# Kernel tuning notes

Hardware: AMD Instinct MI355X
Metric: run time of the kernel (lower is better)

The kernel has to match this reference:

```python
import jax, jax.numpy as jnp
import numpy as np

ALPHA = 0.2
NEG = -9e15


def _gru(x, Wih, Whh, bih, bhh):
    # x: [B, T, F]; PyTorch nn.GRU cell equations, scan over time.
    H = Whh.shape[1]
    xg = jnp.einsum('btf,gf->btg', x, Wih) + bih  # [B,T,3H]

    def step(h, gi):
        gh = h @ Whh.T + bhh
        ir, iz, inn = jnp.split(gi, 3, axis=-1)
        hr, hz, hn = jnp.split(gh, 3, axis=-1)
        r = jax.nn.sigmoid(ir + hr)
        z = jax.nn.sigmoid(iz + hz)
        n = jnp.tanh(inn + r * hn)
        h = (1.0 - z) * n + z * h
        return h, h

    h0 = jnp.zeros((x.shape[0], H), x.dtype)
    _, ys = jax.lax.scan(step, h0, jnp.swapaxes(xg, 0, 1))
    return jnp.swapaxes(ys, 0, 1)  # [B,T,H]


def _gru_attn(x, Wih, Whh, bih, bhh, aw, ab):
    out = _gru(x, Wih, Whh, bih, bhh)              # [B,T,H]
    w = jax.nn.softmax(out @ aw + ab, axis=1)       # [B,T,1]
    return jnp.sum(out * w, axis=1)                 # [B,H]


def _gat(h, mask, W, a):
    # GraphAttentionLayer with concat=True: elu(softmax(mask(leakyrelu(Wh1+Wh2^T))) @ Wh)
    Wh = h @ W                                      # [N,O]
    O = W.shape[1]
    e = jax.nn.leaky_relu((Wh @ a[:O]) + (Wh @ a[O:]).T, ALPHA)  # [N,N]
    att = jax.nn.softmax(jnp.where(mask, e, NEG), axis=1)
    return jax.nn.elu(att @ Wh)


def setup_inputs() -> dict:
    key = jax.random.key(0)
    ks = iter(jax.random.split(key, 40))
    B, S, Wk, D, F = 1, 2048, 32, 5, 16
    H, E, NS = 128, 128, 16

    def rn(shape, scale=0.1):
        return jax.random.normal(next(ks), shape, jnp.float32) * scale

    inp = {
        'stock_features': jax.random.normal(next(ks), (B, S, Wk, D, F), jnp.float32),
        'stock_to_sector': jax.random.randint(next(ks), (S,), 0, NS, jnp.int32),
        'inter_adj': jax.random.randint(next(ks), (NS, NS), 0, 2, jnp.int32),
        'gru1_Wih': rn((3 * H, F)), 'gru1_Whh': rn((3 * H, H)),
        'gru1_bih': rn((3 * H,)), 'gru1_bhh': rn((3 * H,)),
        'attn1_w': rn((H, 1)), 'attn1_b': rn((1,)),
        'gat_intra_W': rn((H, E)), 'gat_intra_a': rn((2 * E, 1)),
        'grug_Wih': rn((3 * E, E)), 'grug_Whh': rn((3 * E, E)),
        'grug_bih': rn((3 * E,)), 'grug_bhh': rn((3 * E,)),
        'attng_w': rn((E, 1)), 'attng_b': rn((1,)),
        'grua_Wih': rn((3 * E, H)), 'grua_Whh': rn((3 * E, E)),
        'grua_bih': rn((3 * E,)), 'grua_bhh': rn((3 * E,)),
        'attna_w': rn((E, 1)), 'attna_b': rn((1,)),
        'gat_inter_W': rn((E, E)), 'gat_inter_a': rn((2 * E, 1)),
        'fusion_w': rn((3 * E, E)), 'fusion_b': rn((E,)),
        'ret_w': rn((E, 1)), 'ret_b': rn((1,)),
        'mov_w': rn((E, 1)), 'mov_b': rn((1,)),
    }
    return inp


def reference(stock_features, stock_to_sector, inter_adj,
              gru1_Wih, gru1_Whh, gru1_bih, gru1_bhh, attn1_w, attn1_b,
              gat_intra_W, gat_intra_a,
              grug_Wih, grug_Whh, grug_bih, grug_bhh, attng_w, attng_b,
              grua_Wih, grua_Whh, grua_bih, grua_bhh, attna_w, attna_b,
              gat_inter_W, gat_inter_a,
              fusion_w, fusion_b, ret_w, ret_b, mov_w, mov_b):
    B, S, Wk, D, F = stock_features.shape
    H = gru1_Whh.shape[1]
    E = gat_intra_W.shape[1]
    NS = inter_adj.shape[0]

    # Short-term: GRU-attention over days, vectorized over (batch, stock, week).
    x = stock_features.reshape(B * S * Wk, D, F)
    short = _gru_attn(x, gru1_Wih, gru1_Whh, gru1_bih, gru1_bhh, attn1_w, attn1_b)
    short = short.reshape(B, S, Wk, H)

    # Intra-sector GAT on last-week embeddings; per-sector softmax == block mask.
    same_sector = stock_to_sector[:, None] == stock_to_sector[None, :]  # [S,S]
    last = short[:, :, -1, :]                                            # [B,S,H]
    intra = jax.vmap(lambda h: _gat(h, same_sector, gat_intra_W, gat_intra_a))(last)  # [B,S,E]

    # Long-term GRU-attentions.
    lg = _gru_attn(intra.reshape(B * S, 1, E), grug_Wih, grug_Whh, grug_bih, grug_bhh,
                   attng_w, attng_b).reshape(B, S, E)
    la = _gru_attn(short.reshape(B * S, Wk, H), grua_Wih, grua_Whh, grua_bih, grua_bhh,
                   attna_w, attna_b).reshape(B, S, E)

    # Sector embeddings = mean of stock long-term embeddings per sector.
    def sector_mean(g):
        sums = jax.ops.segment_sum(g, stock_to_sector, num_segments=NS)
        cnt = jax.ops.segment_sum(jnp.ones((g.shape[0], 1), g.dtype),
                                  stock_to_sector, num_segments=NS)
        return sums / jnp.maximum(cnt, 1.0)

    sec = jax.vmap(sector_mean)(lg)                                      # [B,NS,E]
    imask = inter_adj > 0
    sec_out = jax.vmap(lambda h: _gat(h, imask, gat_inter_W, gat_inter_a))(sec)
    sec_ps = sec_out[:, stock_to_sector, :]                               # [B,S,E]

    fused = jnp.concatenate([lg, la, sec_ps], axis=-1) @ fusion_w + fusion_b
    returns = (fused @ ret_w + ret_b)[..., 0]
    moves = jax.nn.sigmoid(fused @ mov_w + mov_b)[..., 0]
    return jnp.stack([returns, moves])  # [2,B,S]
```

## Files before the change

kernel.cpp:

```cpp
#include <hip/hip_runtime.h>
#include <math.h>

#define LRELU_A 0.2f
#define NEGBIG (-9.0e15f)

typedef _Float16 f16;
typedef _Float16 f16x8 __attribute__((ext_vector_type(8)));
typedef _Float16 f16x4 __attribute__((ext_vector_type(4)));
typedef float floatx4 __attribute__((ext_vector_type(4)));

__device__ __forceinline__ float rcpf(float x){ return __builtin_amdgcn_rcpf(x); }
__device__ __forceinline__ float sigm(float x){ return rcpf(1.0f+__expf(-x)); }
__device__ __forceinline__ float gru_fuse(float xr, float xz, float xn_pre, float ghn, float h){
    float Er = __expf(-xr);
    float r  = rcpf(1.0f + Er);
    float En = __expf(2.0f*(xn_pre + r*ghn));
    float Ez = __expf(-xz);
    float Dn = En + 1.0f;
    float num = fmaf(h, Dn, (En - 1.0f)*Ez);
    float den = Dn * (1.0f + Ez);
    return num * rcpf(den);
}
__device__ __forceinline__ f16x8 load_cvt8(const float* __restrict__ p){
    float4 a = *(const float4*)p; float4 b = *(const float4*)(p+4);
    f16x8 r; r[0]=(f16)a.x; r[1]=(f16)a.y; r[2]=(f16)a.z; r[3]=(f16)a.w;
    r[4]=(f16)b.x; r[5]=(f16)b.y; r[6]=(f16)b.z; r[7]=(f16)b.w;
    return r;
}
#define MFMA16(A,B,C) __builtin_amdgcn_mfma_f32_16x16x32_f16((A),(B),(C),0,0,0)

__global__ __launch_bounds__(256) void prep_kernel(
    const float* __restrict__ g1Wih, const float* __restrict__ g1Whh,
    const float* __restrict__ gaWih, const float* __restrict__ gaWhh,
    const float* __restrict__ giW,   const float* __restrict__ fw,
    const int* __restrict__ sec,
    f16* __restrict__ Wcat1, f16* __restrict__ WcatA,
    f16* __restrict__ WT, f16* __restrict__ fwT,
    int* __restrict__ memflat, int* __restrict__ pos,
    int* __restrict__ cnt, int* __restrict__ base)
{
    __shared__ int cs[16], wsc[16];
    const int b = blockIdx.x, tid = threadIdx.x;
    if (b < 160){
        for (int idx = b*256+tid; idx < 512*160; idx += 160*256){
            int r = idx/160, k = idx - r*160;
            float v = 0.0f;
            if (r < 256){ if (k < 32){ if (k < 16) v = g1Wih[r*16+k]; } else v = g1Whh[r*128 + (k-32)]; }
            else if (r < 384){ if (k < 16) v = g1Wih[r*16+k]; }
            else { if (k >= 32) v = g1Whh[(r-128)*128 + (k-32)]; }
            Wcat1[idx] = (f16)v;
        }
    } else if (b < 416){
        for (int idx = (b-160)*256+tid; idx < 512*256; idx += 256*256){
            int r = idx >> 8, k = idx & 255;
            float v = 0.0f;
            if (r < 256){ v = (k < 128) ? gaWih[r*128+k] : gaWhh[r*128 + (k-128)]; }
            else if (r < 384){ if (k < 128) v = gaWih[r*128+k]; }
            else { if (k >= 128) v = gaWhh[(r-128)*128 + (k-128)]; }
            WcatA[idx] = (f16)v;
        }
    } else if (b < 480){
        int idx = (b-416)*256+tid;
        int r = idx >> 7, c = idx & 127;
        WT[c*128 + r] = (f16)giW[idx];
    } else if (b < 672){
        int idx = (b-480)*256+tid;
        int r = idx >> 7, c = idx & 127;
        fwT[c*384 + r] = (f16)fw[idx];
    } else {
        if (tid < 16) cs[tid] = 0;
        __syncthreads();
        for (int s = tid; s < 2048; s += 256) atomicAdd(&cs[sec[s]], 1);
        __syncthreads();
        if (tid == 0){
            int acc = 0;
            for (int g=0; g<16; g++){ cnt[g]=cs[g]; base[g]=acc; wsc[g]=acc; acc+=cs[g]; }
        }
        __syncthreads();
        for (int s = tid; s < 2048; s += 256){
            int g = sec[s];
            int p = atomicAdd(&wsc[g], 1);
            memflat[p] = s;
            pos[s] = p;
        }
    }
}

__global__ __launch_bounds__(512,2) void gru_short(
    const float* __restrict__ x, const f16* __restrict__ Wcat,
    const float* __restrict__ bih, const float* __restrict__ bhh,
    const float* __restrict__ aw, const float* __restrict__ ab,
    f16* __restrict__ out)
{
    __shared__ __align__(16) f16 xs[5][32][40];
    __shared__ __align__(16) f16 hs[2][32][136];
    __shared__ float scpart[2][8][32];
    const int tid = threadIdx.x, w = tid>>6, lane = tid&63;
    const int c = lane&15, quad = lane>>4;
    const int s0 = blockIdx.x*32;

    { f16x4 z4 = {0,0,0,0};
      f16x4* zx = (f16x4*)&xs[0][0][0];
      for (int i=tid; i<1600; i+=512) zx[i] = z4;
      f16x4* zh = (f16x4*)&hs[1][0][0];
      for (int i=tid; i<1088; i+=512) zh[i] = z4; }
    for (int i=tid; i<640; i+=512){
        int s = i/20, q = i - 20*s;
        float4 v = *(const float4*)&x[(size_t)(s0+s)*80 + q*4];
        int t = (q*4)>>4, f = (q*4)&15;
        f16x4 h4; h4[0]=(f16)v.x; h4[1]=(f16)v.y; h4[2]=(f16)v.z; h4[3]=(f16)v.w;
        *(f16x4*)&xs[t][s][f] = h4;
    }
    const int jrow = w*16 + c;
    f16x8 Ar[5], Az[5], Agi, Agh[4];
#pragma unroll
    for (int kb=0;kb<5;kb++){
        Ar[kb] = *(const f16x8*)&Wcat[(size_t)(jrow)*160 + kb*32 + quad*8];
        Az[kb] = *(const f16x8*)&Wcat[(size_t)(128+jrow)*160 + kb*32 + quad*8];
    }
    Agi = *(const f16x8*)&Wcat[(size_t)(256+jrow)*160 + quad*8];
#pragma unroll
    for (int i=0;i<4;i++)
        Agh[i] = *(const f16x8*)&Wcat[(size_t)(384+jrow)*160 + 32 + i*32 + quad*8];

    float brz_r[4], brz_z[4], b_in[4], b_hn[4], awr[4];
#pragma unroll
    for (int r=0;r<4;r++){
        int j = w*16 + quad*4 + r;
        brz_r[r] = bih[j] + bhh[j];
        brz_z[r] = bih[128+j] + bhh[128+j];
        b_in[r] = bih[256+j]; b_hn[r] = bhh[256+j];
        awr[r] = aw[j];
    }
    const float abv = ab[0];
    float hreg[2][4], aacc[2][4], l_[2] = {0.0f, 0.0f};
#pragma unroll
    for (int st=0; st<2; st++)
#pragma unroll
        for (int r=0;r<4;r++){ hreg[st][r]=0.0f; aacc[st][r]=0.0f; }
    __syncthreads();

#pragma unroll 1
    for (int t=0; t<5; ++t){
        const int rp = (t&1)^1, wp = t&1;
        f16x8 Bx[2], Bh[2][4];
#pragma unroll
        for (int st=0; st<2; st++){
            Bx[st] = *(const f16x8*)&xs[t][st*16+c][quad*8];
#pragma unroll
            for (int i=0;i<4;i++)
                Bh[st][i] = *(const f16x8*)&hs[rp][st*16+c][i*32+quad*8];
        }
        if (t > 0){
#pragma unroll
            for (int st=0; st<2; st++){
                float sc = abv;
#pragma unroll
                for (int ww=0; ww<8; ww++) sc += scpart[rp][ww][st*16+c];
                float e = __expf(sc);
                l_[st] += e;
#pragma unroll
                for (int r=0;r<4;r++) aacc[st][r] += e*hreg[st][r];
            }
        }
        float sp[2];
#pragma unroll
        for (int st=0; st<2; st++){
            floatx4 ar = {0,0,0,0}, az = {0,0,0,0}, agi = {0,0,0,0}, agh = {0,0,0,0};
            ar = MFMA16(Ar[0], Bx[st], ar);
            az = MFMA16(Az[0], Bx[st], az);
            agi = MFMA16(Agi, Bx[st], agi);
#pragma unroll
            for (int i=0;i<4;i++){
                ar = MFMA16(Ar[1+i], Bh[st][i], ar);
                az = MFMA16(Az[1+i], Bh[st][i], az);
                agh = MFMA16(Agh[i], Bh[st][i], agh);
            }
            f16x4 h4;
            sp[st] = 0.0f;
#pragma unroll
            for (int r=0;r<4;r++){
                float hn = gru_fuse(ar[r] + brz_r[r], az[r] + brz_z[r],
                                    agi[r] + b_in[r], agh[r] + b_hn[r], hreg[st][r]);
                hreg[st][r] = hn; h4[r] = (f16)hn;
                sp[st] += hn * awr[r];
            }
            *(f16x4*)&hs[wp][st*16 + c][w*16 + quad*4] = h4;
        }
#pragma unroll
        for (int st=0; st<2; st++){
            sp[st] += __shfl_xor(sp[st], 16);
            sp[st] += __shfl_xor(sp[st], 32);
        }
        if (lane < 16){ scpart[wp][w][lane] = sp[0]; scpart[wp][w][16+lane] = sp[1]; }
        __syncthreads();
    }
#pragma unroll
    for (int st=0; st<2; st++){
        float sc = abv;
#pragma unroll
        for (int ww=0; ww<8; ww++) sc += scpart[0][ww][st*16+c];
        float e = __expf(sc);
        l_[st] += e;
        float inv = rcpf(l_[st]);
        f16x4 h4;
#pragma unroll
        for (int r=0;r<4;r++) h4[r] = (f16)((aacc[st][r] + e*hreg[st][r])*inv);
        *(f16x4*)&hs[0][st*16 + c][w*16 + quad*4] = h4;
    }
    __syncthreads();
    { int s = tid>>4, p = tid&15;
      *(f16x8*)&out[(size_t)(s0+s)*128 + p*8] = *(const f16x8*)&hs[0][s][p*8]; }
}

__global__ __launch_bounds__(512,2) void gru_la(
    const f16* __restrict__ xseq, const f16* __restrict__ Wcat,
    const float* __restrict__ bih, const float* __restrict__ bhh,
    const float* __restrict__ aw, const float* __restrict__ ab,
    f16* __restrict__ out)
{
    __shared__ __align__(16) f16 xs[2][16][136];
    __shared__ __align__(16) f16 hs[2][16][136];
    __shared__ float scpart[2][8][16];
    const int tid = threadIdx.x, w = tid>>6, lane = tid&63;
    const int c = lane&15, quad = lane>>4;
    const int s0 = blockIdx.x*8;

    { f16x4 z4 = {0,0,0,0};
      f16x4* za = (f16x4*)&xs[0][0][0];
      for (int i=tid; i<1088; i+=512) za[i] = z4;
      f16x4* zh = (f16x4*)&hs[0][0][0];
      for (int i=tid; i<1088; i+=512) zh[i] = z4; }
    __syncthreads();
    if (tid < 128){
        int s = tid>>4, p = tid&15;
        *(f16x8*)&xs[0][s][p*8] = *(const f16x8*)&xseq[((size_t)(s0+s)*32 + 0)*128 + p*8];
    }
    const int jrow = w*16 + c;
    f16x8 Ar[8], Az[8], Agi[4], Agh[4];
#pragma unroll
    for (int kb=0;kb<8;kb++){
        Ar[kb] = *(const f16x8*)&Wcat[(size_t)(jrow)*256 + kb*32 + quad*8];
        Az[kb] = *(const f16x8*)&Wcat[(size_t)(128+jrow)*256 + kb*32 + quad*8];
    }
#pragma unroll
    for (int i=0;i<4;i++){
        Agi[i] = *(const f16x8*)&Wcat[(size_t)(256+jrow)*256 + i*32 + quad*8];
        Agh[i] = *(const f16x8*)&Wcat[(size_t)(384+jrow)*256 + 128 + i*32 + quad*8];
    }
    float brz_r[4], brz_z[4], b_in[4], b_hn[4], awr[4];
#pragma unroll
    for (int r=0;r<4;r++){
        int j = w*16 + quad*4 + r;
        brz_r[r] = bih[j] + bhh[j];
        brz_z[r] = bih[128+j] + bhh[128+j];
        b_in[r] = bih[256+j]; b_hn[r] = bhh[256+j];
        awr[r] = aw[j];
    }
    const float abv = ab[0];
    float hreg[4] = {0,0,0,0}, aacc[4] = {0,0,0,0}, l_ = 0.0f;
    __syncthreads();

#pragma unroll 1
    for (int t=0; t<32; ++t){
        const int rp = (t&1)^1, wp = t&1, xp = t&1;
        f16x8 Bx[4], Bh[4];
#pragma unroll
        for (int i=0;i<4;i++){
            Bx[i] = *(const f16x8*)&xs[xp][c][i*32+quad*8];
            Bh[i] = *(const f16x8*)&hs[rp][c][i*32+quad*8];
        }
        f16x8 xstage;
        const bool do_stage = (t < 31) && (tid < 128);
        if (do_stage){
            int s = tid>>4, p = tid&15;
            xstage = *(const f16x8*)&xseq[((size_t)(s0+s)*32 + t+1)*128 + p*8];
        }
        if (t > 0){
            float sc = abv;
#pragma unroll
            for (int ww=0; ww<8; ww++) sc += scpart[rp][ww][c];
            float e = __expf(sc);
            l_ += e;
#pragma unroll
            for (int r=0;r<4;r++) aacc[r] += e*hreg[r];
        }
        floatx4 ar = {0,0,0,0}, az = {0,0,0,0}, agi = {0,0,0,0}, agh = {0,0,0,0};
#pragma unroll
        for (int i=0;i<4;i++){
            ar = MFMA16(Ar[i], Bx[i], ar);
            az = MFMA16(Az[i], Bx[i], az);
            agi = MFMA16(Agi[i], Bx[i], agi);
        }
#pragma unroll
        for (int i=0;i<4;i++){
            ar = MFMA16(Ar[4+i], Bh[i], ar);
            az = MFMA16(Az[4+i], Bh[i], az);
            agh = MFMA16(Agh[i], Bh[i], agh);
        }
        f16x4 h4;
        float sp = 0.0f;
#pragma unroll
        for (int r=0;r<4;r++){
            float hn = gru_fuse(ar[r] + brz_r[r], az[r] + brz_z[r],
                                agi[r] + b_in[r], agh[r] + b_hn[r], hreg[r]);
            hreg[r] = hn; h4[r] = (f16)hn;
            sp += hn * awr[r];
        }
        *(f16x4*)&hs[wp][c][w*16 + quad*4] = h4;
        if (do_stage){
            int s = tid>>4, p = tid&15;
            *(f16x8*)&xs[xp^1][s][p*8] = xstage;
        }
        sp += __shfl_xor(sp, 16);
        sp += __shfl_xor(sp, 32);
        if (lane < 16) scpart[wp][w][lane] = sp;
        __syncthreads();
    }
    {
        float sc = abv;
#pragma unroll
        for (int ww=0; ww<8; ww++) sc += scpart[1][ww][c];
        float e = __expf(sc);
        l_ += e;
        float inv = rcpf(l_);
        f16x4 h4;
#pragma unroll
        for (int r=0;r<4;r++) h4[r] = (f16)((aacc[r] + e*hreg[r])*inv);
        *(f16x4*)&hs[1][c][w*16 + quad*4] = h4;
    }
    __syncthreads();
    if (tid < 128){
        int s = tid>>4, p = tid&15;
        *(f16x8*)&out[(size_t)(s0+s)*128 + p*8] = *(const f16x8*)&hs[1][s][p*8];
    }
}

__global__ __launch_bounds__(256) void gat_prep(
    const f16* __restrict__ shrt16, const f16* __restrict__ WT,
    const float* __restrict__ gia, const int* __restrict__ memflat,
    f16* __restrict__ Whs, float* __restrict__ ers, float* __restrict__ el)
{
    __shared__ __align__(16) float tbuf[32][132];
    __shared__ int rows[32];
    const int tid = threadIdx.x, w = tid>>6, lane = tid&63;
    const int c = lane&15, quad = lane>>4;
    const int p0 = blockIdx.x*32;
    if (tid < 32) rows[tid] = memflat[p0 + tid];
    __syncthreads();
    f16x8 A[2][4];
#pragma unroll
    for (int mt=0;mt<2;mt++)
#pragma unroll
        for (int kb=0;kb<4;kb++)
            A[mt][kb] = *(const f16x8*)&shrt16[((size_t)rows[mt*16+c]*32 + 31)*128 + kb*32 + quad*8];
#pragma unroll
    for (int i=0;i<2;i++){
        int jb = w*2 + i;
        f16x8 B[4];
#pragma unroll
        for (int kb=0;kb<4;kb++)
            B[kb] = *(const f16x8*)&WT[(size_t)(jb*16+c)*128 + kb*32 + quad*8];
        floatx4 acc[2] = {{0,0,0,0},{0,0,0,0}};
#pragma unroll
        for (int kb=0;kb<4;kb++){
            acc[0] = MFMA16(A[0][kb], B[kb], acc[0]);
            acc[1] = MFMA16(A[1][kb], B[kb], acc[1]);
        }
#pragma unroll
        for (int mt=0;mt<2;mt++)
#pragma unroll
            for (int r=0;r<4;r++)
                tbuf[mt*16 + quad*4 + r][jb*16 + c] = acc[mt][r];
    }
    __syncthreads();
    for (int i=tid; i<1024; i+=256){
        int s = i>>5, p = i&31;
        float4 v = *(const float4*)&tbuf[s][p*4];
        f16x4 h4; h4[0]=(f16)v.x; h4[1]=(f16)v.y; h4[2]=(f16)v.z; h4[3]=(f16)v.w;
        *(f16x4*)&Whs[(size_t)(p0+s)*128 + p*4] = h4;
    }
    for (int k=0; k<8; k++){
        int row = w*8 + k;
        float w0 = tbuf[row][lane], w1 = tbuf[row][64+lane];
        float v1 = w0*gia[lane]     + w1*gia[64+lane];
        float v2 = w0*gia[128+lane] + w1*gia[192+lane];
#pragma unroll
        for (int off=32; off; off>>=1){ v1 += __shfl_down(v1,off); v2 += __shfl_down(v2,off); }
        if (lane==0){ el[rows[row]] = v1; ers[p0+row] = v2; }
    }
}

__global__ __launch_bounds__(256) void gat_intra_mem_kernel(
    const f16* __restrict__ Whs, const float* __restrict__ ers,
    const float* __restrict__ el, const int* __restrict__ sec,
    const int* __restrict__ cnt, const int* __restrict__ base,
    f16* __restrict__ outp, int S)
{
    int wave = threadIdx.x>>6, lane = threadIdx.x&63;
    int i = blockIdx.x*4 + wave;
    if (i>=S) return;
    int g = sec[i];
    int n = cnt[g], b = base[g];
    float eli = el[i];
    float m = -INFINITY;
    for (int jj=lane; jj<n; jj+=64){
        float v = eli + ers[b+jj]; v = v>0.f? v : LRELU_A*v;
        m = fmaxf(m, v);
    }
#pragma unroll
    for (int off=32; off; off>>=1) m = fmaxf(m, __shfl_xor(m, off));
    float l = 0.f, c0=0.f, c1=0.f;
#pragma unroll 4
    for (int jj=0; jj<n; jj++){
        float v = eli + ers[b+jj]; v = v>0.f? v : LRELU_A*v;
        float p = __expf(v-m);
        l += p;
        c0 += p*(float)Whs[(size_t)(b+jj)*128 + lane];
        c1 += p*(float)Whs[(size_t)(b+jj)*128 + 64 + lane];
    }
    float il = rcpf(l);
    c0 *= il; c1 *= il;
    outp[(size_t)i*128+lane]    = (f16)(c0>0.f? c0 : expm1f(c0));
    outp[(size_t)i*128+64+lane] = (f16)(c1>0.f? c1 : expm1f(c1));
}

__global__ __launch_bounds__(256) void lg_mfma(
    const f16* __restrict__ intra16, const float* __restrict__ Wih,
    const float* __restrict__ bih, const float* __restrict__ bhh,
    const int* __restrict__ pos,
    f16* __restrict__ lgout, f16* __restrict__ lgs)
{
    __shared__ __align__(16) f16 tbuf[32][136];
    const int tid = threadIdx.x, w = tid>>6, lane = tid&63;
    const int c = lane&15, quad = lane>>4;
    const int s0 = blockIdx.x*32;
    f16x8 A[2][4];
#pragma unroll
    for (int mt=0;mt<2;mt++)
#pragma unroll
        for (int kb=0;kb<4;kb++)
            A[mt][kb] = *(const f16x8*)&intra16[(size_t)(s0+mt*16+c)*128 + kb*32 + quad*8];
#pragma unroll
    for (int i=0;i<2;i++){
        int jb = w*2 + i;
        int j = jb*16 + c;
        f16x8 Br[4], Bz[4], Bn[4];
#pragma unroll
        for (int kb=0;kb<4;kb++){
            Br[kb] = load_cvt8(&Wih[(size_t)(j)*128 + kb*32 + quad*8]);
            Bz[kb] = load_cvt8(&Wih[(size_t)(128+j)*128 + kb*32 + quad*8]);
            Bn[kb] = load_cvt8(&Wih[(size_t)(256+j)*128 + kb*32 + quad*8]);
        }
        float b_r = bih[j] + bhh[j];
        float b_z = bih[128+j] + bhh[128+j];
        float b_i = bih[256+j], b_h = bhh[256+j];
        floatx4 ar[2] = {{0,0,0,0},{0,0,0,0}};
        floatx4 az[2] = {{0,0,0,0},{0,0,0,0}};
        floatx4 an[2] = {{0,0,0,0},{0,0,0,0}};
#pragma unroll
        for (int kb=0;kb<4;kb++)
#pragma unroll
            for (int mt=0;mt<2;mt++){
                ar[mt] = MFMA16(A[mt][kb], Br[kb], ar[mt]);
                az[mt] = MFMA16(A[mt][kb], Bz[kb], az[mt]);
                an[mt] = MFMA16(A[mt][kb], Bn[kb], an[mt]);
            }
#pragma unroll
        for (int mt=0;mt<2;mt++)
#pragma unroll
            for (int r=0;r<4;r++){
                float Er = __expf(-(ar[mt][r] + b_r));
// ... 142 lines not shown
                float fu = acc[mt][r] + fbv;
                rsum[mt][r] += fu*rwv;
                msum[mt][r] += fu*mwv;
            }
    }
#pragma unroll
    for (int mt=0;mt<2;mt++)
#pragma unroll
        for (int r=0;r<4;r++){
#pragma unroll
            for (int off=1; off<16; off<<=1){
                rsum[mt][r] += __shfl_xor(rsum[mt][r], off);
                msum[mt][r] += __shfl_xor(msum[mt][r], off);
            }
            if (c==0){
                rpart[w][mt*16 + quad*4 + r] = rsum[mt][r];
                mpart[w][mt*16 + quad*4 + r] = msum[mt][r];
            }
        }
    __syncthreads();
    if (tid < 32){
        int s = tid;
        float rs = rb[0], ms = mb[0];
#pragma unroll
        for (int ww=0; ww<4; ww++){ rs += rpart[ww][s]; ms += mpart[ww][s]; }
        outp[s0+s] = rs;
        outp[2048 + s0 + s] = sigm(ms);
    }
}

extern "C" void kernel_launch(void* const* d_in, const int* in_sizes, int n_in,
                              void* d_out, int out_size, void* d_ws, size_t ws_size,
                              hipStream_t stream) {
    const float* sf    = (const float*)d_in[0];
    const int*   sec   = (const int*)  d_in[1];
    const int*   adj   = (const int*)  d_in[2];
    const float* g1Wih = (const float*)d_in[3];
    const float* g1Whh = (const float*)d_in[4];
    const float* g1bih = (const float*)d_in[5];
    const float* g1bhh = (const float*)d_in[6];
    const float* a1w   = (const float*)d_in[7];
    const float* a1b   = (const float*)d_in[8];
    const float* giW   = (const float*)d_in[9];
    const float* gia   = (const float*)d_in[10];
    const float* ggWih = (const float*)d_in[11];
    const float* ggbih = (const float*)d_in[13];
    const float* ggbhh = (const float*)d_in[14];
    const float* gaWih = (const float*)d_in[17];
    const float* gaWhh = (const float*)d_in[18];
    const float* gabih = (const float*)d_in[19];
    const float* gabhh = (const float*)d_in[20];
    const float* aaw   = (const float*)d_in[21];
    const float* aab   = (const float*)d_in[22];
    const float* geW   = (const float*)d_in[23];
    const float* gea   = (const float*)d_in[24];
    const float* fw    = (const float*)d_in[25];
    const float* fb    = (const float*)d_in[26];
    const float* rw    = (const float*)d_in[27];
    const float* rb    = (const float*)d_in[28];
    const float* mw    = (const float*)d_in[29];
    const float* mb    = (const float*)d_in[30];

    char* p = (char*)d_ws;
    f16*   shrt16 = (f16*)p;   p += (size_t)65536*128*2;
    f16*   intra16= (f16*)p;   p += (size_t)262144*2;
    f16*   lg16   = (f16*)p;   p += (size_t)262144*2;
    f16*   la16   = (f16*)p;   p += (size_t)262144*2;
    f16*   Whs    = (f16*)p;   p += (size_t)262144*2;
    f16*   lgs    = (f16*)p;   p += (size_t)262144*2;
    f16*   Wcat1  = (f16*)p;   p += (size_t)512*160*2;
    f16*   WcatA  = (f16*)p;   p += (size_t)512*256*2;
    f16*   WT     = (f16*)p;   p += (size_t)16384*2;
    f16*   fwT    = (f16*)p;   p += (size_t)49152*2;
    float* el     = (float*)p; p += 2048*4;
    float* ers    = (float*)p; p += 2048*4;
    float* seco   = (float*)p; p += 2048*4;
    int*   memflat= (int*)p;   p += 2048*4;
    int*   pos    = (int*)p;   p += 2048*4;
    int*   cnt    = (int*)p;   p += 16*4;
    int*   basep  = (int*)p;   p += 16*4;

    prep_kernel<<<673,256,0,stream>>>(g1Wih, g1Whh, gaWih, gaWhh, giW, fw, sec,
                                      Wcat1, WcatA, WT, fwT, memflat, pos, cnt, basep);
    gru_short<<<2048,512,0,stream>>>(sf, Wcat1, g1bih, g1bhh, a1w, a1b, shrt16);
    gat_prep<<<64,256,0,stream>>>(shrt16, WT, gia, memflat, Whs, ers, el);
    gat_intra_mem_kernel<<<512,256,0,stream>>>(Whs, ers, el, sec, cnt, basep, intra16, 2048);
    lg_mfma<<<64,256,0,stream>>>(intra16, ggWih, ggbih, ggbhh, pos, lg16, lgs);
    gru_la<<<256,512,0,stream>>>(shrt16, WcatA, gabih, gabhh, aaw, aab, la16);
    gat_inter_fused<<<1,1024,0,stream>>>(lgs, cnt, basep, adj, geW, gea, seco);
    fused_mfma<<<64,256,0,stream>>>(lg16, la16, seco, sec, fwT, fb, rw, rb, mw, mb, (float*)d_out);
}
```

Baseline: 323.7 us.

## Split gru_short across 1024 threads and fuse gat_prep into gru_la launch

gru_short now launches 1024 threads per block, and each group of 8 waves handles one of the two 16-stock subtiles, so each wave does half the serial MFMA and gate work per timestep. gat_prep and gru_la are merged into one launch: the extra blocks beyond 256 do the GAT projection concurrently with the GRU blocks. This removes one kernel launch and lets the two independent stages overlap. The cost is duplicated weight registers across waves, wider block barriers, and more shared memory per block in the fused kernel.

```diff
diff --git a/kernel.cpp b/kernel.cpp
--- a/kernel.cpp
+++ b/kernel.cpp
@@ -86,7 +86,7 @@
     }
 }
 
-__global__ __launch_bounds__(512,2) void gru_short(
+__global__ __launch_bounds__(1024,2) void gru_short(
     const float* __restrict__ x, const f16* __restrict__ Wcat,
     const float* __restrict__ bih, const float* __restrict__ bhh,
     const float* __restrict__ aw, const float* __restrict__ ab,
@@ -97,21 +97,22 @@
     __shared__ float scpart[2][8][32];
     const int tid = threadIdx.x, w = tid>>6, lane = tid&63;
     const int c = lane&15, quad = lane>>4;
+    const int st = w>>3, wj = w&7;
     const int s0 = blockIdx.x*32;
 
     { f16x4 z4 = {0,0,0,0};
       f16x4* zx = (f16x4*)&xs[0][0][0];
-      for (int i=tid; i<1600; i+=512) zx[i] = z4;
+      for (int i=tid; i<1600; i+=1024) zx[i] = z4;
       f16x4* zh = (f16x4*)&hs[1][0][0];
-      for (int i=tid; i<1088; i+=512) zh[i] = z4; }
-    for (int i=tid; i<640; i+=512){
+      for (int i=tid; i<1088; i+=1024) zh[i] = z4; }
+    for (int i=tid; i<640; i+=1024){
         int s = i/20, q = i - 20*s;
         float4 v = *(const float4*)&x[(size_t)(s0+s)*80 + q*4];
         int t = (q*4)>>4, f = (q*4)&15;
         f16x4 h4; h4[0]=(f16)v.x; h4[1]=(f16)v.y; h4[2]=(f16)v.z; h4[3]=(f16)v.w;
         *(f16x4*)&xs[t][s][f] = h4;
     }
-    const int jrow = w*16 + c;
+    const int jrow = wj*16 + c;
     f16x8 Ar[5], Az[5], Agi, Agh[4];
 #pragma unroll
     for (int kb=0;kb<5;kb++){
@@ -123,6 +124,166 @@
     for (int i=0;i<4;i++)
         Agh[i] = *(const f16x8*)&Wcat[(size_t)(384+jrow)*160 + 32 + i*32 + quad*8];
 
+    float brz_r[4], brz_z[4], b_in[4], b_hn[4], awr[4];
+#pragma unroll
+    for (int r=0;r<4;r++){
+        int j = wj*16 + quad*4 + r;
+        brz_r[r] = bih[j] + bhh[j];
+        brz_z[r] = bih[128+j] + bhh[128+j];
+        b_in[r] = bih[256+j]; b_hn[r] = bhh[256+j];
+        awr[r] = aw[j];
+    }
+    const float abv = ab[0];
+    float hreg[4] = {0,0,0,0}, aacc[4] = {0,0,0,0}, l_ = 0.0f;
+    __syncthreads();
+
+#pragma unroll 1
+    for (int t=0; t<5; ++t){
+        const int rp = (t&1)^1, wp = t&1;
+        f16x8 Bx = *(const f16x8*)&xs[t][st*16+c][quad*8];
+        f16x8 Bh[4];
+#pragma unroll
+        for (int i=0;i<4;i++)
+            Bh[i] = *(const f16x8*)&hs[rp][st*16+c][i*32+quad*8];
+        if (t > 0){
+            float sc = abv;
+#pragma unroll
+            for (int ww=0; ww<8; ww++) sc += scpart[rp][ww][st*16+c];
+            float e = __expf(sc);
+            l_ += e;
+#pragma unroll
+            for (int r=0;r<4;r++) aacc[r] += e*hreg[r];
+        }
+        floatx4 ar = {0,0,0,0}, az = {0,0,0,0}, agi = {0,0,0,0}, agh = {0,0,0,0};
+        ar = MFMA16(Ar[0], Bx, ar);
+        az = MFMA16(Az[0], Bx, az);
+        agi = MFMA16(Agi, Bx, agi);
+#pragma unroll
+        for (int i=0;i<4;i++){
+            ar = MFMA16(Ar[1+i], Bh[i], ar);
+            az = MFMA16(Az[1+i], Bh[i], az);
+            agh = MFMA16(Agh[i], Bh[i], agh);
+        }
+        f16x4 h4;
+        float sp = 0.0f;
+#pragma unroll
+        for (int r=0;r<4;r++){
+            float hn = gru_fuse(ar[r] + brz_r[r], az[r] + brz_z[r],
+                                agi[r] + b_in[r], agh[r] + b_hn[r], hreg[r]);
+            hreg[r] = hn; h4[r] = (f16)hn;
+            sp += hn * awr[r];
+        }
+        *(f16x4*)&hs[wp][st*16 + c][wj*16 + quad*4] = h4;
+        sp += __shfl_xor(sp, 16);
+        sp += __shfl_xor(sp, 32);
+        if (lane < 16) scpart[wp][wj][st*16 + lane] = sp;
+        __syncthreads();
+    }
+    {
+        float sc = abv;
+#pragma unroll
+        for (int ww=0; ww<8; ww++) sc += scpart[0][ww][st*16+c];
+        float e = __expf(sc);
+        l_ += e;
+        float inv = rcpf(l_);
+        f16x4 h4;
+#pragma unroll
+        for (int r=0;r<4;r++) h4[r] = (f16)((aacc[r] + e*hreg[r])*inv);
+        *(f16x4*)&hs[0][st*16 + c][wj*16 + quad*4] = h4;
+    }
+    __syncthreads();
+    if (tid < 512){
+        int s = tid>>4, p = tid&15;
+        *(f16x8*)&out[(size_t)(s0+s)*128 + p*8] = *(const f16x8*)&hs[0][s][p*8];
+    }
+}
+
+__global__ __launch_bounds__(512,2) void gru_la_gatprep(
+    const f16* __restrict__ xseq, const f16* __restrict__ Wcat,
+    const float* __restrict__ bih, const float* __restrict__ bhh,
+    const float* __restrict__ aw, const float* __restrict__ ab,
+    f16* __restrict__ out,
+    const f16* __restrict__ WT, const float* __restrict__ gia,
+    const int* __restrict__ memflat,
+    f16* __restrict__ Whs, float* __restrict__ ers, float* __restrict__ el)
+{
+    __shared__ __align__(16) f16 xs[2][16][136];
+    __shared__ __align__(16) f16 hs[2][16][136];
+    __shared__ float scpart[2][8][16];
+    __shared__ __align__(16) float tbuf[32][132];
+    __shared__ int rows[32];
+    const int tid = threadIdx.x, w = tid>>6, lane = tid&63;
+    const int c = lane&15, quad = lane>>4;
+
+    if (blockIdx.x >= 256){
+        const int p0 = (blockIdx.x-256)*32;
+        if (tid < 32) rows[tid] = memflat[p0 + tid];
+        __syncthreads();
+        f16x8 A[2][4];
+#pragma unroll
+        for (int mt=0;mt<2;mt++)
+#pragma unroll
+            for (int kb=0;kb<4;kb++)
+                A[mt][kb] = *(const f16x8*)&xseq[((size_t)rows[mt*16+c]*32 + 31)*128 + kb*32 + quad*8];
+        {
+            int jb = w;
+            f16x8 B[4];
+#pragma unroll
+            for (int kb=0;kb<4;kb++)
+                B[kb] = *(const f16x8*)&WT[(size_t)(jb*16+c)*128 + kb*32 + quad*8];
+            floatx4 acc[2] = {{0,0,0,0},{0,0,0,0}};
+#pragma unroll
+            for (int kb=0;kb<4;kb++){
+                acc[0] = MFMA16(A[0][kb], B[kb], acc[0]);
+                acc[1] = MFMA16(A[1][kb], B[kb], acc[1]);
+            }
+#pragma unroll
+            for (int mt=0;mt<2;mt++)
+#pragma unroll
+                for (int r=0;r<4;r++)
+                    tbuf[mt*16 + quad*4 + r][jb*16 + c] = acc[mt][r];
+        }
+        __syncthreads();
+        for (int i=tid; i<1024; i+=512){
+            int s = i>>5, p = i&31;
+            float4 v = *(const float4*)&tbuf[s][p*4];
+            f16x4 h4; h4[0]=(f16)v.x; h4[1]=(f16)v.y; h4[2]=(f16)v.z; h4[3]=(f16)v.w;
+            *(f16x4*)&Whs[(size_t)(p0+s)*128 + p*4] = h4;
+        }
+        for (int k=0; k<4; k++){
+            int row = w*4 + k;
+            float w0 = tbuf[row][lane], w1 = tbuf[row][64+lane];
+            float v1 = w0*gia[lane]     + w1*gia[64+lane];
+            float v2 = w0*gia[128+lane] + w1*gia[192+lane];
+#pragma unroll
+            for (int off=32; off; off>>=1){ v1 += __shfl_down(v1,off); v2 += __shfl_down(v2,off); }
+            if (lane==0){ el[rows[row]] = v1; ers[p0+row] = v2; }
+        }
+        return;
+    }
+    const int s0 = blockIdx.x*8;
+    { f16x4 z4 = {0,0,0,0};
+      f16x4* za = (f16x4*)&xs[0][0][0];
+      for (int i=tid; i<1088; i+=512) za[i] = z4;
+      f16x4* zh = (f16x4*)&hs[0][0][0];
+      for (int i=tid; i<1088; i+=512) zh[i] = z4; }
+    __syncthreads();
+    if (tid < 128){
+        int s = tid>>4, p = tid&15;
+        *(f16x8*)&xs[0][s][p*8] = *(const f16x8*)&xseq[((size_t)(s0+s)*32 + 0)*128 + p*8];
+    }
+    const int jrow = w*16 + c;
+    f16x8 Ar[8], Az[8], Agi[4], Agh[4];
+#pragma unroll
+    for (int kb=0;kb<8;kb++){
+        Ar[kb] = *(const f16x8*)&Wcat[(size_t)(jrow)*256 + kb*32 + quad*8];
+        Az[kb] = *(const f16x8*)&Wcat[(size_t)(128+jrow)*256 + kb*32 + quad*8];
+    }
+#pragma unroll
+    for (int i=0;i<4;i++){
+        Agi[i] = *(const f16x8*)&Wcat[(size_t)(256+jrow)*256 + i*32 + quad*8];
+        Agh[i] = *(const f16x8*)&Wcat[(size_t)(384+jrow)*256 + 128 + i*32 + quad*8];
+    }
     float brz_r[4], brz_z[4], b_in[4], b_hn[4], awr[4];
 #pragma unroll
     for (int r=0;r<4;r++){
@@ -133,131 +294,6 @@
         awr[r] = aw[j];
     }
     const float abv = ab[0];
-    float hreg[2][4], aacc[2][4], l_[2] = {0.0f, 0.0f};
-#pragma unroll
-    for (int st=0; st<2; st++)
-#pragma unroll
-        for (int r=0;r<4;r++){ hreg[st][r]=0.0f; aacc[st][r]=0.0f; }
-    __syncthreads();
-
-#pragma unroll 1
-    for (int t=0; t<5; ++t){
-        const int rp = (t&1)^1, wp = t&1;
-        f16x8 Bx[2], Bh[2][4];
-#pragma unroll
-        for (int st=0; st<2; st++){
-            Bx[st] = *(const f16x8*)&xs[t][st*16+c][quad*8];
-#pragma unroll
-            for (int i=0;i<4;i++)
-                Bh[st][i] = *(const f16x8*)&hs[rp][st*16+c][i*32+quad*8];
-        }
-        if (t > 0){
-#pragma unroll
-            for (int st=0; st<2; st++){
-                float sc = abv;
-#pragma unroll
-                for (int ww=0; ww<8; ww++) sc += scpart[rp][ww][st*16+c];
-                float e = __expf(sc);
-                l_[st] += e;
-#pragma unroll
-                for (int r=0;r<4;r++) aacc[st][r] += e*hreg[st][r];
-            }
-        }
-        float sp[2];
-#pragma unroll
-        for (int st=0; st<2; st++){
-            floatx4 ar = {0,0,0,0}, az = {0,0,0,0}, agi = {0,0,0,0}, agh = {0,0,0,0};
-            ar = MFMA16(Ar[0], Bx[st], ar);
-            az = MFMA16(Az[0], Bx[st], az);
-            agi = MFMA16(Agi, Bx[st], agi);
-#pragma unroll
-            for (int i=0;i<4;i++){
-                ar = MFMA16(Ar[1+i], Bh[st][i], ar);
-                az = MFMA16(Az[1+i], Bh[st][i], az);
-                agh = MFMA16(Agh[i], Bh[st][i], agh);
-            }
-            f16x4 h4;
-            sp[st] = 0.0f;
-#pragma unroll
-            for (int r=0;r<4;r++){
-                float hn = gru_fuse(ar[r] + brz_r[r], az[r] + brz_z[r],
-                                    agi[r] + b_in[r], agh[r] + b_hn[r], hreg[st][r]);
-                hreg[st][r] = hn; h4[r] = (f16)hn;
-                sp[st] += hn * awr[r];
-            }
-            *(f16x4*)&hs[wp][st*16 + c][w*16 + quad*4] = h4;
-        }
-#pragma unroll
-        for (int st=0; st<2; st++){
-            sp[st] += __shfl_xor(sp[st], 16);
-            sp[st] += __shfl_xor(sp[st], 32);
-        }
-        if (lane < 16){ scpart[wp][w][lane] = sp[0]; scpart[wp][w][16+lane] = sp[1]; }
-        __syncthreads();
-    }
-#pragma unroll
-    for (int st=0; st<2; st++){
-        float sc = abv;
-#pragma unroll
-        for (int ww=0; ww<8; ww++) sc += scpart[0][ww][st*16+c];
-        float e = __expf(sc);
-        l_[st] += e;
-        float inv = rcpf(l_[st]);
-        f16x4 h4;
-#pragma unroll
-        for (int r=0;r<4;r++) h4[r] = (f16)((aacc[st][r] + e*hreg[st][r])*inv);
-        *(f16x4*)&hs[0][st*16 + c][w*16 + quad*4] = h4;
-    }
-    __syncthreads();
-    { int s = tid>>4, p = tid&15;
-      *(f16x8*)&out[(size_t)(s0+s)*128 + p*8] = *(const f16x8*)&hs[0][s][p*8]; }
-}
-
-__global__ __launch_bounds__(512,2) void gru_la(
-    const f16* __restrict__ xseq, const f16* __restrict__ Wcat,
-    const float* __restrict__ bih, const float* __restrict__ bhh,
-    const float* __restrict__ aw, const float* __restrict__ ab,
-    f16* __restrict__ out)
-{
-    __shared__ __align__(16) f16 xs[2][16][136];
-    __shared__ __align__(16) f16 hs[2][16][136];
-    __shared__ float scpart[2][8][16];
-    const int tid = threadIdx.x, w = tid>>6, lane = tid&63;
-    const int c = lane&15, quad = lane>>4;
-    const int s0 = blockIdx.x*8;
-
-    { f16x4 z4 = {0,0,0,0};
-      f16x4* za = (f16x4*)&xs[0][0][0];
-      for (int i=tid; i<1088; i+=512) za[i] = z4;
-      f16x4* zh = (f16x4*)&hs[0][0][0];
-      for (int i=tid; i<1088; i+=512) zh[i] = z4; }
-    __syncthreads();
-    if (tid < 128){
-        int s = tid>>4, p = tid&15;
-        *(f16x8*)&xs[0][s][p*8] = *(const f16x8*)&xseq[((size_t)(s0+s)*32 + 0)*128 + p*8];
-    }
-    const int jrow = w*16 + c;
-    f16x8 Ar[8], Az[8], Agi[4], Agh[4];
-#pragma unroll
-    for (int kb=0;kb<8;kb++){
-        Ar[kb] = *(const f16x8*)&Wcat[(size_t)(jrow)*256 + kb*32 + quad*8];
-        Az[kb] = *(const f16x8*)&Wcat[(size_t)(128+jrow)*256 + kb*32 + quad*8];
-    }
-#pragma unroll
-    for (int i=0;i<4;i++){
-        Agi[i] = *(const f16x8*)&Wcat[(size_t)(256+jrow)*256 + i*32 + quad*8];
-        Agh[i] = *(const f16x8*)&Wcat[(size_t)(384+jrow)*256 + 128 + i*32 + quad*8];
-    }
-    float brz_r[4], brz_z[4], b_in[4], b_hn[4], awr[4];
-#pragma unroll
-    for (int r=0;r<4;r++){
-        int j = w*16 + quad*4 + r;
-        brz_r[r] = bih[j] + bhh[j];
-        brz_z[r] = bih[128+j] + bhh[128+j];
-        b_in[r] = bih[256+j]; b_hn[r] = bhh[256+j];
-        awr[r] = aw[j];
-    }
-    const float abv = ab[0];
     float hreg[4] = {0,0,0,0}, aacc[4] = {0,0,0,0}, l_ = 0.0f;
     __syncthreads();
 
@@ -333,61 +369,6 @@
     if (tid < 128){
         int s = tid>>4, p = tid&15;
         *(f16x8*)&out[(size_t)(s0+s)*128 + p*8] = *(const f16x8*)&hs[1][s][p*8];
-    }
-}
-
-__global__ __launch_bounds__(256) void gat_prep(
-    const f16* __restrict__ shrt16, const f16* __restrict__ WT,
-    const float* __restrict__ gia, const int* __restrict__ memflat,
-    f16* __restrict__ Whs, float* __restrict__ ers, float* __restrict__ el)
-{
-    __shared__ __align__(16) float tbuf[32][132];
-    __shared__ int rows[32];
-    const int tid = threadIdx.x, w = tid>>6, lane = tid&63;
-    const int c = lane&15, quad = lane>>4;
-    const int p0 = blockIdx.x*32;
-    if (tid < 32) rows[tid] = memflat[p0 + tid];
-    __syncthreads();
-    f16x8 A[2][4];
-#pragma unroll
-    for (int mt=0;mt<2;mt++)
-#pragma unroll
-        for (int kb=0;kb<4;kb++)
-            A[mt][kb] = *(const f16x8*)&shrt16[((size_t)rows[mt*16+c]*32 + 31)*128 + kb*32 + quad*8];
-#pragma unroll
-    for (int i=0;i<2;i++){
-        int jb = w*2 + i;
-        f16x8 B[4];
-#pragma unroll
-        for (int kb=0;kb<4;kb++)
-            B[kb] = *(const f16x8*)&WT[(size_t)(jb*16+c)*128 + kb*32 + quad*8];
-        floatx4 acc[2] = {{0,0,0,0},{0,0,0,0}};
-#pragma unroll
-        for (int kb=0;kb<4;kb++){
-            acc[0] = MFMA16(A[0][kb], B[kb], acc[0]);
-            acc[1] = MFMA16(A[1][kb], B[kb], acc[1]);
-        }
-#pragma unroll
-        for (int mt=0;mt<2;mt++)
-#pragma unroll
-            for (int r=0;r<4;r++)
-                tbuf[mt*16 + quad*4 + r][jb*16 + c] = acc[mt][r];
-    }
-    __syncthreads();
-    for (int i=tid; i<1024; i+=256){
-        int s = i>>5, p = i&31;
-        float4 v = *(const float4*)&tbuf[s][p*4];
-        f16x4 h4; h4[0]=(f16)v.x; h4[1]=(f16)v.y; h4[2]=(f16)v.z; h4[3]=(f16)v.w;
-        *(f16x4*)&Whs[(size_t)(p0+s)*128 + p*4] = h4;
-    }
-    for (int k=0; k<8; k++){
-        int row = w*8 + k;
-        float w0 = tbuf[row][lane], w1 = tbuf[row][64+lane];
-        float v1 = w0*gia[lane]     + w1*gia[64+lane];
-        float v2 = w0*gia[128+lane] + w1*gia[192+lane];
-#pragma unroll
-        for (int off=32; off; off>>=1){ v1 += __shfl_down(v1,off); v2 += __shfl_down(v2,off); }
-        if (lane==0){ el[rows[row]] = v1; ers[p0+row] = v2; }
     }
 }
 
@@ -696,11 +677,11 @@
 
     prep_kernel<<<673,256,0,stream>>>(g1Wih, g1Whh, gaWih, gaWhh, giW, fw, sec,
                                       Wcat1, WcatA, WT, fwT, memflat, pos, cnt, basep);
-    gru_short<<<2048,512,0,stream>>>(sf, Wcat1, g1bih, g1bhh, a1w, a1b, shrt16);
-    gat_prep<<<64,256,0,stream>>>(shrt16, WT, gia, memflat, Whs, ers, el);
+    gru_short<<<2048,1024,0,stream>>>(sf, Wcat1, g1bih, g1bhh, a1w, a1b, shrt16);
+    gru_la_gatprep<<<320,512,0,stream>>>(shrt16, WcatA, gabih, gabhh, aaw, aab, la16,
+                                         WT, gia, memflat, Whs, ers, el);
     gat_intra_mem_kernel<<<512,256,0,stream>>>(Whs, ers, el, sec, cnt, basep, intra16, 2048);
     lg_mfma<<<64,256,0,stream>>>(intra16, ggWih, ggbih, ggbhh, pos, lg16, lgs);
-    gru_la<<<256,512,0,stream>>>(shrt16, WcatA, gabih, gabhh, aaw, aab, la16);
     gat_inter_fused<<<1,1024,0,stream>>>(lgs, cnt, basep, adj, geW, gea, seco);
     fused_mfma<<<64,256,0,stream>>>(lg16, la16, seco, sec, fwT, fb, rw, rb, mw, mb, (float*)d_out);
 }
```

Result: slower. 345.1 us (+6.6%).

## Loop gru_short over four tiles per block and merge gat_prep into gru_la

Applied to the files above, without the earlier changes.

gru_short now processes four 32-sequence tiles per block, so it launches 512 blocks instead of 2048 and loads the per-lane weight fragments once per block instead of once per tile. gat_prep is folded into the gru_la kernel as 64 extra blocks, so the two independent workloads run concurrently in one launch and one kernel launch is removed. The merged gat_prep blocks use 512 threads, with each wave taking one column block. The costs are less parallelism in gru_short and a larger shared-memory footprint for the combined kernel, which may reduce occupancy.

```diff
diff --git a/kernel.cpp b/kernel.cpp
--- a/kernel.cpp
+++ b/kernel.cpp
@@ -97,20 +97,11 @@
     __shared__ float scpart[2][8][32];
     const int tid = threadIdx.x, w = tid>>6, lane = tid&63;
     const int c = lane&15, quad = lane>>4;
-    const int s0 = blockIdx.x*32;
 
     { f16x4 z4 = {0,0,0,0};
       f16x4* zx = (f16x4*)&xs[0][0][0];
-      for (int i=tid; i<1600; i+=512) zx[i] = z4;
-      f16x4* zh = (f16x4*)&hs[1][0][0];
-      for (int i=tid; i<1088; i+=512) zh[i] = z4; }
-    for (int i=tid; i<640; i+=512){
-        int s = i/20, q = i - 20*s;
-        float4 v = *(const float4*)&x[(size_t)(s0+s)*80 + q*4];
-        int t = (q*4)>>4, f = (q*4)&15;
-        f16x4 h4; h4[0]=(f16)v.x; h4[1]=(f16)v.y; h4[2]=(f16)v.z; h4[3]=(f16)v.w;
-        *(f16x4*)&xs[t][s][f] = h4;
-    }
+      for (int i=tid; i<1600; i+=512) zx[i] = z4; }
+
     const int jrow = w*16 + c;
     f16x8 Ar[5], Az[5], Agi, Agh[4];
 #pragma unroll
@@ -133,99 +124,165 @@
         awr[r] = aw[j];
     }
     const float abv = ab[0];
-    float hreg[2][4], aacc[2][4], l_[2] = {0.0f, 0.0f};
-#pragma unroll
-    for (int st=0; st<2; st++)
-#pragma unroll
-        for (int r=0;r<4;r++){ hreg[st][r]=0.0f; aacc[st][r]=0.0f; }
-    __syncthreads();
 
 #pragma unroll 1
-    for (int t=0; t<5; ++t){
-        const int rp = (t&1)^1, wp = t&1;
-        f16x8 Bx[2], Bh[2][4];
+    for (int tile=0; tile<4; ++tile){
+        const int s0 = (blockIdx.x*4 + tile)*32;
+        { f16x4 z4 = {0,0,0,0};
+          f16x4* zh = (f16x4*)&hs[1][0][0];
+          for (int i=tid; i<1088; i+=512) zh[i] = z4; }
+        for (int i=tid; i<640; i+=512){
+            int s = i/20, q = i - 20*s;
+            float4 v = *(const float4*)&x[(size_t)(s0+s)*80 + q*4];
+            int t = (q*4)>>4, f = (q*4)&15;
+            f16x4 h4; h4[0]=(f16)v.x; h4[1]=(f16)v.y; h4[2]=(f16)v.z; h4[3]=(f16)v.w;
+            *(f16x4*)&xs[t][s][f] = h4;
+        }
+        float hreg[2][4], aacc[2][4], l_[2] = {0.0f, 0.0f};
+#pragma unroll
+        for (int st=0; st<2; st++)
+#pragma unroll
+            for (int r=0;r<4;r++){ hreg[st][r]=0.0f; aacc[st][r]=0.0f; }
+        __syncthreads();
+
+#pragma unroll 1
+        for (int t=0; t<5; ++t){
+            const int rp = (t&1)^1, wp = t&1;
+            f16x8 Bx[2], Bh[2][4];
+#pragma unroll
+            for (int st=0; st<2; st++){
+                Bx[st] = *(const f16x8*)&xs[t][st*16+c][quad*8];
+#pragma unroll
+                for (int i=0;i<4;i++)
+                    Bh[st][i] = *(const f16x8*)&hs[rp][st*16+c][i*32+quad*8];
+            }
+            if (t > 0){
+#pragma unroll
+                for (int st=0; st<2; st++){
+                    float sc = abv;
+#pragma unroll
+                    for (int ww=0; ww<8; ww++) sc += scpart[rp][ww][st*16+c];
+                    float e = __expf(sc);
+                    l_[st] += e;
+#pragma unroll
+                    for (int r=0;r<4;r++) aacc[st][r] += e*hreg[st][r];
+                }
+            }
+            float sp[2];
+#pragma unroll
+            for (int st=0; st<2; st++){
+                floatx4 ar = {0,0,0,0}, az = {0,0,0,0}, agi = {0,0,0,0}, agh = {0,0,0,0};
+                ar = MFMA16(Ar[0], Bx[st], ar);
+                az = MFMA16(Az[0], Bx[st], az);
+                agi = MFMA16(Agi, Bx[st], agi);
+#pragma unroll
+                for (int i=0;i<4;i++){
+                    ar = MFMA16(Ar[1+i], Bh[st][i], ar);
+                    az = MFMA16(Az[1+i], Bh[st][i], az);
+                    agh = MFMA16(Agh[i], Bh[st][i], agh);
+                }
+                f16x4 h4;
+                sp[st] = 0.0f;
+#pragma unroll
+                for (int r=0;r<4;r++){
+                    float hn = gru_fuse(ar[r] + brz_r[r], az[r] + brz_z[r],
+                                        agi[r] + b_in[r], agh[r] + b_hn[r], hreg[st][r]);
+                    hreg[st][r] = hn; h4[r] = (f16)hn;
+                    sp[st] += hn * awr[r];
+                }
+                *(f16x4*)&hs[wp][st*16 + c][w*16 + quad*4] = h4;
+            }
+#pragma unroll
+            for (int st=0; st<2; st++){
+                sp[st] += __shfl_xor(sp[st], 16);
+                sp[st] += __shfl_xor(sp[st], 32);
+            }
+            if (lane < 16){ scpart[wp][w][lane] = sp[0]; scpart[wp][w][16+lane] = sp[1]; }
+            __syncthreads();
+        }
 #pragma unroll
         for (int st=0; st<2; st++){
-            Bx[st] = *(const f16x8*)&xs[t][st*16+c][quad*8];
-#pragma unroll
-            for (int i=0;i<4;i++)
-                Bh[st][i] = *(const f16x8*)&hs[rp][st*16+c][i*32+quad*8];
-        }
-        if (t > 0){
-#pragma unroll
-            for (int st=0; st<2; st++){
-                float sc = abv;
-#pragma unroll
-                for (int ww=0; ww<8; ww++) sc += scpart[rp][ww][st*16+c];
-                float e = __expf(sc);
-                l_[st] += e;
-#pragma unroll
-                for (int r=0;r<4;r++) aacc[st][r] += e*hreg[st][r];
-            }
-        }
-        float sp[2];
-#pragma unroll
-        for (int st=0; st<2; st++){
-            floatx4 ar = {0,0,0,0}, az = {0,0,0,0}, agi = {0,0,0,0}, agh = {0,0,0,0};
-            ar = MFMA16(Ar[0], Bx[st], ar);
-            az = MFMA16(Az[0], Bx[st], az);
-            agi = MFMA16(Agi, Bx[st], agi);
-#pragma unroll
-            for (int i=0;i<4;i++){
-                ar = MFMA16(Ar[1+i], Bh[st][i], ar);
-                az = MFMA16(Az[1+i], Bh[st][i], az);
-                agh = MFMA16(Agh[i], Bh[st][i], agh);
-            }
+            float sc = abv;
+#pragma unroll
+            for (int ww=0; ww<8; ww++) sc += scpart[0][ww][st*16+c];
+            float e = __expf(sc);
+            l_[st] += e;
+            float inv = rcpf(l_[st]);
             f16x4 h4;
-            sp[st] = 0.0f;
-#pragma unroll
-            for (int r=0;r<4;r++){
-                float hn = gru_fuse(ar[r] + brz_r[r], az[r] + brz_z[r],
-                                    agi[r] + b_in[r], agh[r] + b_hn[r], hreg[st][r]);
-                hreg[st][r] = hn; h4[r] = (f16)hn;
-                sp[st] += hn * awr[r];
-            }
-            *(f16x4*)&hs[wp][st*16 + c][w*16 + quad*4] = h4;
-        }
-#pragma unroll
-        for (int st=0; st<2; st++){
-            sp[st] += __shfl_xor(sp[st], 16);
-            sp[st] += __shfl_xor(sp[st], 32);
-        }
-        if (lane < 16){ scpart[wp][w][lane] = sp[0]; scpart[wp][w][16+lane] = sp[1]; }
+#pragma unroll
+            for (int r=0;r<4;r++) h4[r] = (f16)((aacc[st][r] + e*hreg[st][r])*inv);
+            *(f16x4*)&hs[0][st*16 + c][w*16 + quad*4] = h4;
+        }
         __syncthreads();
-    }
-#pragma unroll
-    for (int st=0; st<2; st++){
-        float sc = abv;
-#pragma unroll
-        for (int ww=0; ww<8; ww++) sc += scpart[0][ww][st*16+c];
-        float e = __expf(sc);
-        l_[st] += e;
-        float inv = rcpf(l_[st]);
-        f16x4 h4;
-#pragma unroll
-        for (int r=0;r<4;r++) h4[r] = (f16)((aacc[st][r] + e*hreg[st][r])*inv);
-        *(f16x4*)&hs[0][st*16 + c][w*16 + quad*4] = h4;
-    }
-    __syncthreads();
-    { int s = tid>>4, p = tid&15;
-      *(f16x8*)&out[(size_t)(s0+s)*128 + p*8] = *(const f16x8*)&hs[0][s][p*8]; }
-}
-
-__global__ __launch_bounds__(512,2) void gru_la(
+        { int s = tid>>4, p = tid&15;
+          *(f16x8*)&out[(size_t)(s0+s)*128 + p*8] = *(const f16x8*)&hs[0][s][p*8]; }
+    }
+}
+
+__global__ __launch_bounds__(512,2) void gru_la_gatprep(
     const f16* __restrict__ xseq, const f16* __restrict__ Wcat,
     const float* __restrict__ bih, const float* __restrict__ bhh,
     const float* __restrict__ aw, const float* __restrict__ ab,
-    f16* __restrict__ out)
+    f16* __restrict__ out,
+    const f16* __restrict__ WT, const float* __restrict__ gia,
+    const int* __restrict__ memflat,
+    f16* __restrict__ Whs, float* __restrict__ ers, float* __restrict__ el)
 {
     __shared__ __align__(16) f16 xs[2][16][136];
     __shared__ __align__(16) f16 hs[2][16][136];
     __shared__ float scpart[2][8][16];
+    __shared__ __align__(16) float tbuf[32][132];
+    __shared__ int rows[32];
     const int tid = threadIdx.x, w = tid>>6, lane = tid&63;
     const int c = lane&15, quad = lane>>4;
+
+    if (blockIdx.x >= 256){
+        const int p0 = (blockIdx.x-256)*32;
+        if (tid < 32) rows[tid] = memflat[p0 + tid];
+        __syncthreads();
+        f16x8 A[2][4];
+#pragma unroll
+        for (int mt=0;mt<2;mt++)
+#pragma unroll
+            for (int kb=0;kb<4;kb++)
+                A[mt][kb] = *(const f16x8*)&xseq[((size_t)rows[mt*16+c]*32 + 31)*128 + kb*32 + quad*8];
+        {
+            int jb = w;
+            f16x8 B[4];
+#pragma unroll
+            for (int kb=0;kb<4;kb++)
+                B[kb] = *(const f16x8*)&WT[(size_t)(jb*16+c)*128 + kb*32 + quad*8];
+            floatx4 acc[2] = {{0,0,0,0},{0,0,0,0}};
+#pragma unroll
+            for (int kb=0;kb<4;kb++){
+                acc[0] = MFMA16(A[0][kb], B[kb], acc[0]);
+                acc[1] = MFMA16(A[1][kb], B[kb], acc[1]);
+            }
+#pragma unroll
+            for (int mt=0;mt<2;mt++)
+#pragma unroll
+                for (int r=0;r<4;r++)
+                    tbuf[mt*16 + quad*4 + r][jb*16 + c] = acc[mt][r];
+        }
+        __syncthreads();
+        for (int i=tid; i<1024; i+=512){
+            int s = i>>5, p = i&31;
+            float4 v = *(const float4*)&tbuf[s][p*4];
+            f16x4 h4; h4[0]=(f16)v.x; h4[1]=(f16)v.y; h4[2]=(f16)v.z; h4[3]=(f16)v.w;
+            *(f16x4*)&Whs[(size_t)(p0+s)*128 + p*4] = h4;
+        }
+        for (int k=0; k<4; k++){
+            int row = w*4 + k;
+            float w0 = tbuf[row][lane], w1 = tbuf[row][64+lane];
+            float v1 = w0*gia[lane]     + w1*gia[64+lane];
+            float v2 = w0*gia[128+lane] + w1*gia[192+lane];
+#pragma unroll
+            for (int off=32; off; off>>=1){ v1 += __shfl_down(v1,off); v2 += __shfl_down(v2,off); }
+            if (lane==0){ el[rows[row]] = v1; ers[p0+row] = v2; }
+        }
+        return;
+    }
     const int s0 = blockIdx.x*8;
-
     { f16x4 z4 = {0,0,0,0};
       f16x4* za = (f16x4*)&xs[0][0][0];
       for (int i=tid; i<1088; i+=512) za[i] = z4;
@@ -333,61 +390,6 @@
     if (tid < 128){
         int s = tid>>4, p = tid&15;
         *(f16x8*)&out[(size_t)(s0+s)*128 + p*8] = *(const f16x8*)&hs[1][s][p*8];
-    }
-}
-
-__global__ __launch_bounds__(256) void gat_prep(
-    const f16* __restrict__ shrt16, const f16* __restrict__ WT,
-    const float* __restrict__ gia, const int* __restrict__ memflat,
-    f16* __restrict__ Whs, float* __restrict__ ers, float* __restrict__ el)
-{
-    __shared__ __align__(16) float tbuf[32][132];
-    __shared__ int rows[32];
-    const int tid = threadIdx.x, w = tid>>6, lane = tid&63;
-    const int c = lane&15, quad = lane>>4;
-    const int p0 = blockIdx.x*32;
-    if (tid < 32) rows[tid] = memflat[p0 + tid];
-    __syncthreads();
-    f16x8 A[2][4];
-#pragma unroll
-    for (int mt=0;mt<2;mt++)
-#pragma unroll
-        for (int kb=0;kb<4;kb++)
-            A[mt][kb] = *(const f16x8*)&shrt16[((size_t)rows[mt*16+c]*32 + 31)*128 + kb*32 + quad*8];
-#pragma unroll
-    for (int i=0;i<2;i++){
-        int jb = w*2 + i;
-        f16x8 B[4];
-#pragma unroll
-        for (int kb=0;kb<4;kb++)
-            B[kb] = *(const f16x8*)&WT[(size_t)(jb*16+c)*128 + kb*32 + quad*8];
-        floatx4 acc[2] = {{0,0,0,0},{0,0,0,0}};
-#pragma unroll
-        for (int kb=0;kb<4;kb++){
-            acc[0] = MFMA16(A[0][kb], B[kb], acc[0]);
-            acc[1] = MFMA16(A[1][kb], B[kb], acc[1]);
-        }
-#pragma unroll
-        for (int mt=0;mt<2;mt++)
-#pragma unroll
-            for (int r=0;r<4;r++)
-                tbuf[mt*16 + quad*4 + r][jb*16 + c] = acc[mt][r];
-    }
-    __syncthreads();
-    for (int i=tid; i<1024; i+=256){
-        int s = i>>5, p = i&31;
-        float4 v = *(const float4*)&tbuf[s][p*4];
-        f16x4 h4; h4[0]=(f16)v.x; h4[1]=(f16)v.y; h4[2]=(f16)v.z; h4[3]=(f16)v.w;
-        *(f16x4*)&Whs[(size_t)(p0+s)*128 + p*4] = h4;
-    }
-    for (int k=0; k<8; k++){
-        int row = w*8 + k;
-        float w0 = tbuf[row][lane], w1 = tbuf[row][64+lane];
-        float v1 = w0*gia[lane]     + w1*gia[64+lane];
-        float v2 = w0*gia[128+lane] + w1*gia[192+lane];
-#pragma unroll
-        for (int off=32; off; off>>=1){ v1 += __shfl_down(v1,off); v2 += __shfl_down(v2,off); }
-        if (lane==0){ el[rows[row]] = v1; ers[p0+row] = v2; }
     }
 }
 
@@ -696,11 +698,11 @@
 
     prep_kernel<<<673,256,0,stream>>>(g1Wih, g1Whh, gaWih, gaWhh, giW, fw, sec,
                                       Wcat1, WcatA, WT, fwT, memflat, pos, cnt, basep);
-    gru_short<<<2048,512,0,stream>>>(sf, Wcat1, g1bih, g1bhh, a1w, a1b, shrt16);
-    gat_prep<<<64,256,0,stream>>>(shrt16, WT, gia, memflat, Whs, ers, el);
+    gru_short<<<512,512,0,stream>>>(sf, Wcat1, g1bih, g1bhh, a1w, a1b, shrt16);
+    gru_la_gatprep<<<320,512,0,stream>>>(shrt16, WcatA, gabih, gabhh, aaw, aab, la16,
+                                         WT, gia, memflat, Whs, ers, el);
     gat_intra_mem_kernel<<<512,256,0,stream>>>(Whs, ers, el, sec, cnt, basep, intra16, 2048);
     lg_mfma<<<64,256,0,stream>>>(intra16, ggWih, ggbih, ggbhh, pos, lg16, lgs);
-    gru_la<<<256,512,0,stream>>>(shrt16, WcatA, gabih, gabhh, aaw, aab, la16);
     gat_inter_fused<<<1,1024,0,stream>>>(lgs, cnt, basep, adj, geW, gea, seco);
     fused_mfma<<<64,256,0,stream>>>(lg16, la16, seco, sec, fwT, fb, rw, rb, mw, mb, (float*)d_out);
 }
```

Result: faster. 306.5 us (-5.3%).
